# Performance work log

Measured on AMD Instinct MI355X. Metric: run time of the kernel, lower is better.

The kernel has to match this reference:

```python
import jax, jax.numpy as jnp
import numpy as np

DIM = 768
H = 12
HD = DIM // H
SCALE = HD ** (-0.5)


def setup_inputs() -> dict:
    key = jax.random.key(0)
    ks = jax.random.split(key, 10)
    s = DIM ** (-0.5)
    x = jax.random.normal(ks[0], (8, 1024, DIM), dtype=jnp.float32)
    Wq = jax.random.normal(ks[1], (DIM, DIM), dtype=jnp.float32) * s
    Wk = jax.random.normal(ks[2], (DIM, DIM), dtype=jnp.float32) * s
    Wv = jax.random.normal(ks[3], (DIM, DIM), dtype=jnp.float32) * s
    Wl = jax.random.normal(ks[4], (H, H), dtype=jnp.float32) * (H ** -0.5)
    bl = jax.random.normal(ks[5], (H,), dtype=jnp.float32) * 0.02
    Ww = jax.random.normal(ks[6], (H, H), dtype=jnp.float32) * (H ** -0.5)
    bw = jax.random.normal(ks[7], (H,), dtype=jnp.float32) * 0.02
    Wp = jax.random.normal(ks[8], (DIM, DIM), dtype=jnp.float32) * s
    bp = jax.random.normal(ks[9], (DIM,), dtype=jnp.float32) * 0.02
    return {"x": x, "Wq": Wq, "Wk": Wk, "Wv": Wv, "Wl": Wl, "bl": bl,
            "Ww": Ww, "bw": bw, "Wp": Wp, "bp": bp}


def reference(x, Wq, Wk, Wv, Wl, bl, Ww, bw, Wp, bp):
    B, N, C = x.shape
    # QKV projections (no bias), split heads -> (B, H, N, hd)
    q = (x @ Wq).reshape(B, N, H, HD).transpose(0, 2, 1, 3) * SCALE
    k = (x @ Wk).reshape(B, N, H, HD).transpose(0, 2, 1, 3)
    v = (x @ Wv).reshape(B, N, H, HD).transpose(0, 2, 1, 3)
    # scores: (B, H, N, N)
    attn = jnp.einsum('bhid,bhjd->bhij', q, k)
    # talking heads pre-softmax: mix over head axis (Linear on last dim of BNNH)
    attn = jnp.einsum('bhij,gh->bgij', attn, Wl) + bl[None, :, None, None]
    attn = jax.nn.softmax(attn, axis=-1)
    # talking heads post-softmax
    attn = jnp.einsum('bhij,gh->bgij', attn, Ww) + bw[None, :, None, None]
    out = jnp.einsum('bhij,bhjd->bhid', attn, v)  # (B, H, N, hd)
    out = out.transpose(0, 2, 1, 3).reshape(B, N, C)
    return out @ Wp + bp
```

## Files before the change

### kernel.cpp

```cpp
#include <hip/hip_runtime.h>
#include <hip/hip_bf16.h>

#define DIM 768
#define NH 12
#define HD 64
#define SEQ 1024
#define BATCH 8
#define JSPA 4
#define JSPB 2
#define LOG2E 1.44269504f

typedef __bf16 bf16x8 __attribute__((ext_vector_type(8)));
typedef _Float16 f16x4 __attribute__((ext_vector_type(4)));
typedef _Float16 f16x8 __attribute__((ext_vector_type(8)));
typedef float f32x4 __attribute__((ext_vector_type(4)));

__global__ __launch_bounds__(256) void xcvt(
    const float* __restrict__ X, __bf16* __restrict__ Xb)
{
  const size_t i = ((size_t)blockIdx.x * 256 + threadIdx.x) * 8;
  float4 a0 = *(const float4*)(X + i);
  float4 a1 = *(const float4*)(X + i + 4);
  bf16x8 v = { (__bf16)a0.x, (__bf16)a0.y, (__bf16)a0.z, (__bf16)a0.w,
               (__bf16)a1.x, (__bf16)a1.y, (__bf16)a1.z, (__bf16)a1.w };
  *(bf16x8*)(Xb + i) = v;
}

__global__ __launch_bounds__(256) void wtrans(
    const float* __restrict__ Wq, const float* __restrict__ Wk,
    const float* __restrict__ Wv, const float* __restrict__ Wp,
    __bf16* __restrict__ Tq, __bf16* __restrict__ Tk,
    __bf16* __restrict__ Tv, _Float16* __restrict__ Tp)
{
  const int z = blockIdx.z;
  const float* W = (z==0) ? Wq : (z==1) ? Wk : (z==2) ? Wv : Wp;
  __shared__ float tile[32][33];
  const int t = threadIdx.x, tx = t & 31, ty = t >> 5;
  const int k0 = blockIdx.y * 32, n0 = blockIdx.x * 32;
#pragma unroll
  for (int u = 0; u < 4; ++u)
    tile[ty + u*8][tx] = W[(size_t)(k0 + ty + u*8) * DIM + n0 + tx];
  __syncthreads();
  if (z == 3) {
#pragma unroll
    for (int u = 0; u < 4; ++u)
      Tp[(size_t)(n0 + ty + u*8) * DIM + k0 + tx] = (_Float16)tile[tx][ty + u*8];
  } else {
    __bf16* T = (z==0) ? Tq : (z==1) ? Tk : Tv;
#pragma unroll
    for (int u = 0; u < 4; ++u)
      T[(size_t)(n0 + ty + u*8) * DIM + k0 + tx] = (__bf16)tile[tx][ty + u*8];
  }
}

__global__ __launch_bounds__(256) void gemm_qkv(
    const __bf16* __restrict__ Xb, const __bf16* __restrict__ WT,
    __bf16* __restrict__ Qo, __bf16* __restrict__ Ko, _Float16* __restrict__ Vt2)
{
  __shared__ __bf16 As[128 * 40];
  __shared__ __bf16 Bs[128 * 40];

  const int t = threadIdx.x, lane = t & 63, w = t >> 6;
  const int n16 = lane & 15, q = lane >> 4;
  const int m0 = blockIdx.y * 128, n0 = blockIdx.x * 128;
  const int wm = (w >> 1) * 64, wn = (w & 1) * 64;

  const int srow = t >> 2, scol = (t & 3) * 8;
  const __bf16* Ag = Xb + (size_t)(m0 + srow) * DIM + scol;
  const __bf16* Bg = WT + (size_t)(n0 + srow) * DIM + scol;

  f32x4 acc[4][4];
#pragma unroll
  for (int mt = 0; mt < 4; ++mt)
#pragma unroll
    for (int nt = 0; nt < 4; ++nt) acc[mt][nt] = (f32x4){0.f,0.f,0.f,0.f};

  for (int kb = 0; kb < DIM; kb += 32) {
    __syncthreads();
    bf16x8 a0 = *(const bf16x8*)(Ag + kb);
    bf16x8 a1 = *(const bf16x8*)(Ag + (size_t)64 * DIM + kb);
    bf16x8 b0 = *(const bf16x8*)(Bg + kb);
    bf16x8 b1 = *(const bf16x8*)(Bg + (size_t)64 * DIM + kb);
    *(bf16x8*)&As[srow * 40 + scol] = a0;
    *(bf16x8*)&As[(srow + 64) * 40 + scol] = a1;
    *(bf16x8*)&Bs[srow * 40 + scol] = b0;
    *(bf16x8*)&Bs[(srow + 64) * 40 + scol] = b1;
    __syncthreads();

    bf16x8 af[4], bg[4];
#pragma unroll
    for (int mt = 0; mt < 4; ++mt)
      af[mt] = *(const bf16x8*)&As[(wm + mt*16 + n16) * 40 + q*8];
#pragma unroll
    for (int nt = 0; nt < 4; ++nt)
      bg[nt] = *(const bf16x8*)&Bs[(wn + nt*16 + n16) * 40 + q*8];
#pragma unroll
    for (int mt = 0; mt < 4; ++mt)
#pragma unroll
      for (int nt = 0; nt < 4; ++nt)
        acc[mt][nt] = __builtin_amdgcn_mfma_f32_16x16x32_bf16(af[mt], bg[nt], acc[mt][nt], 0, 0, 0);
  }

#pragma unroll
  for (int nt = 0; nt < 4; ++nt) {
    const int n = n0 + wn + nt*16 + n16;
    const int z = n / DIM, c = n % DIM;
    const int h = c >> 6, d = c & 63;
#pragma unroll
    for (int mt = 0; mt < 4; ++mt) {
#pragma unroll
      for (int r = 0; r < 4; ++r) {
        const int row = m0 + wm + mt*16 + q*4 + r;
        const int bb = row >> 10, ii = row & 1023;
        const float v = acc[mt][nt][r];
        if (z == 0)
          Qo[(((size_t)bb*NH + h)*SEQ + ii)*HD + d] = (__bf16)(v * 0.125f);
        else if (z == 1)
          Ko[(((size_t)bb*NH + h)*SEQ + ii)*HD + d] = (__bf16)v;
        else
          Vt2[((((size_t)bb*NH + h)*64 + (ii >> 4))*HD + d)*16 + (ii & 15)] = (_Float16)v;
      }
    }
  }
}

__global__ __launch_bounds__(256) void attn_sums(
    const __bf16* __restrict__ Qg, const __bf16* __restrict__ Kg,
    const float* __restrict__ Wl, const float* __restrict__ bl,
    float* __restrict__ lpart)
{
  __shared__ _Float16 Sl[2][12][324];

  const int t = threadIdx.x, lane = t & 63, w = t >> 6;
  const int n16 = lane & 15, q = lane >> 4;
  const int h0 = w * 3;
  const int b = blockIdx.x, i0 = blockIdx.y * 16, z = blockIdx.z;
  const int jt0 = z * (SEQ/16/JSPA), jt1 = jt0 + SEQ/16/JSPA;
  const size_t bbase = (size_t)b * NH * SEQ * HD;

  f16x4 wlA;
  f32x4 blC;
#pragma unroll
  for (int j = 0; j < 4; ++j) {
    const int k = q*4 + j;
    wlA[j] = (n16 < 12 && k < 12) ? (_Float16)(Wl[n16*12 + k] * LOG2E) : (_Float16)0.f;
    blC[j] = (k < 12) ? bl[k] * LOG2E : 0.f;
  }

  bf16x8 qf[3][2];
#pragma unroll
  for (int hh = 0; hh < 3; ++hh)
#pragma unroll
    for (int cc = 0; cc < 2; ++cc)
      qf[hh][cc] = *(const bf16x8*)(Qg + bbase + ((size_t)(h0+hh)*SEQ + i0 + n16)*HD + cc*32 + q*8);

  const f32x4 z4 = {0.f, 0.f, 0.f, 0.f};

  float lrun[4][4];
#pragma unroll
  for (int c = 0; c < 4; ++c)
#pragma unroll
    for (int r = 0; r < 4; ++r) lrun[c][r] = 0.f;

  bf16x8 kC[3][2], kN[3][2];
#pragma unroll
  for (int hh = 0; hh < 3; ++hh) {
    const __bf16* kp = Kg + bbase + ((size_t)(h0+hh)*SEQ + jt0*16 + n16)*HD + q*8;
    kC[hh][0] = *(const bf16x8*)kp;
    kC[hh][1] = *(const bf16x8*)(kp + 32);
  }

#pragma unroll 2
  for (int jt = jt0; jt < jt1; ++jt) {
    const int buf = jt & 1;
    const int jn = (jt < jt1 - 1) ? jt + 1 : jt;
#pragma unroll
    for (int hh = 0; hh < 3; ++hh) {
      const __bf16* kp = Kg + bbase + ((size_t)(h0+hh)*SEQ + jn*16 + n16)*HD + q*8;
      kN[hh][0] = *(const bf16x8*)kp;
      kN[hh][1] = *(const bf16x8*)(kp + 32);
    }
#pragma unroll
    for (int hh = 0; hh < 3; ++hh) {
      f32x4 s = __builtin_amdgcn_mfma_f32_16x16x32_bf16(kC[hh][0], qf[hh][0], z4, 0, 0, 0);
      s = __builtin_amdgcn_mfma_f32_16x16x32_bf16(kC[hh][1], qf[hh][1], s, 0, 0, 0);
      f16x4 sh = { (_Float16)s[0], (_Float16)s[1], (_Float16)s[2], (_Float16)s[3] };
      *(f16x4*)&Sl[buf][h0+hh][n16*20 + q*4] = sh;
    }
    __syncthreads();
#pragma unroll
    for (int c = 0; c < 4; ++c) {
      const int i = w*4 + c;
      f16x4 sf;
#pragma unroll
      for (int dd = 0; dd < 4; ++dd) {
        int h = q*4 + dd; if (h > 11) h = 11;
        sf[dd] = Sl[buf][h][i*20 + n16];
      }
      f32x4 sm = __builtin_amdgcn_mfma_f32_16x16x16f16(wlA, sf, blC, 0, 0, 0);
#pragma unroll
      for (int r = 0; r < 4; ++r) lrun[c][r] += __builtin_amdgcn_exp2f(sm[r]);
    }
#pragma unroll
    for (int hh = 0; hh < 3; ++hh) { kC[hh][0] = kN[hh][0]; kC[hh][1] = kN[hh][1]; }
  }

  const int tile = b * (SEQ/16) + blockIdx.y;
#pragma unroll
  for (int c = 0; c < 4; ++c) {
#pragma unroll
    for (int r = 0; r < 4; ++r) {
      float l = lrun[c][r];
      l += __shfl_xor(l, 1);
      l += __shfl_xor(l, 2);
      l += __shfl_xor(l, 4);
      l += __shfl_xor(l, 8);
      const int g = q*4 + r;
      if (n16 == 0 && g < 12)
        lpart[(((size_t)tile*JSPA + z)*12 + g)*16 + w*4 + c] = l;
    }
  }
}

__global__ __launch_bounds__(256) void attn_pv(
    const __bf16* __restrict__ Qg, const __bf16* __restrict__ Kg,
    const _Float16* __restrict__ Vt2,
    const float* __restrict__ Wl, const float* __restrict__ bl,
    const float* __restrict__ Ww, const float* __restrict__ bw,
    const float* __restrict__ lpart,
    _Float16* __restrict__ Ap0, _Float16* __restrict__ Ap1)
{
  __shared__ _Float16 Sl[2][12][324];
  __shared__ _Float16 Pl[2][16 * 248];

  const int t = threadIdx.x, lane = t & 63, w = t >> 6;
  const int n16 = lane & 15, q = lane >> 4;
  const int h0 = w * 3;
  const int b = blockIdx.x, i0 = blockIdx.y * 16, z = blockIdx.z;
  const int jt0 = z * (SEQ/16/JSPB), jt1 = jt0 + SEQ/16/JSPB;
  const size_t bbase = (size_t)b * NH * SEQ * HD;

  f16x4 wlA, wwA;
  f32x4 blC, bwC;
#pragma unroll
  for (int j = 0; j < 4; ++j) {
    const int k = q*4 + j;
    wlA[j] = (n16 < 12 && k < 12) ? (_Float16)(Wl[n16*12 + k] * LOG2E) : (_Float16)0.f;
    wwA[j] = (n16 < 12 && k < 12) ? (_Float16)Ww[n16*12 + k] : (_Float16)0.f;
    blC[j] = (k < 12) ? bl[k] * LOG2E : 0.f;
    bwC[j] = (k < 12) ? bw[k] : 0.f;
  }

  const int tile = b * (SEQ/16) + blockIdx.y;
  float linv[4][4];
#pragma unroll
  for (int c = 0; c < 4; ++c)
#pragma unroll
    for (int r = 0; r < 4; ++r) {
      const int g = q*4 + r;
      if (g < 12) {
        float l = 0.f;
#pragma unroll
        for (int zz = 0; zz < JSPA; ++zz)
          l += lpart[(((size_t)tile*JSPA + zz)*12 + g)*16 + w*4 + c];
        linv[c][r] = 1.0f / l;
      } else {
        linv[c][r] = 0.f;
      }
    }

  bf16x8 qf[3][2];
#pragma unroll
  for (int hh = 0; hh < 3; ++hh)
#pragma unroll
    for (int cc = 0; cc < 2; ++cc)
      qf[hh][cc] = *(const bf16x8*)(Qg + bbase + ((size_t)(h0+hh)*SEQ + i0 + n16)*HD + cc*32 + q*8);

  const f32x4 z4 = {0.f, 0.f, 0.f, 0.f};

  f32x4 oacc[3][4];
#pragma unroll
  for (int hh = 0; hh < 3; ++hh)
#pragma unroll
    for (int dc = 0; dc < 4; ++dc) oacc[hh][dc] = z4;

  bf16x8 kC[3][2], kN[3][2];
  f16x4 vC[3][4], vN[3][4];
#pragma unroll
  for (int hh = 0; hh < 3; ++hh) {
    const __bf16* kp = Kg + bbase + ((size_t)(h0+hh)*SEQ + jt0*16 + n16)*HD + q*8;
    kC[hh][0] = *(const bf16x8*)kp;
    kC[hh][1] = *(const bf16x8*)(kp + 32);
  }

#pragma unroll 2
  for (int jt = jt0; jt < jt1; ++jt) {
    const int buf = jt & 1;
    const int jn = (jt < jt1 - 1) ? jt + 1 : jt;
#pragma unroll
    for (int hh = 0; hh < 3; ++hh) {
      const __bf16* kp = Kg + bbase + ((size_t)(h0+hh)*SEQ + jn*16 + n16)*HD + q*8;
      kN[hh][0] = *(const bf16x8*)kp;
      kN[hh][1] = *(const bf16x8*)(kp + 32);
    }
#pragma unroll
    for (int hh = 0; hh < 3; ++hh) {
      const _Float16* vb = Vt2 + (((size_t)(b*NH + h0 + hh)*64 + jt)*HD)*16;
#pragma unroll
      for (int dc = 0; dc < 4; ++dc)
        vN[hh][dc] = *(const f16x4*)(vb + (size_t)(dc*16 + n16)*16 + q*4);
    }
#pragma unroll
    for (int hh = 0; hh < 3; ++hh) {
      f32x4 s = __builtin_amdgcn_mfma_f32_16x16x32_bf16(kC[hh][0], qf[hh][0], z4, 0, 0, 0);
      s = __builtin_amdgcn_mfma_f32_16x16x32_bf16(kC[hh][1], qf[hh][1], s, 0, 0, 0);
      f16x4 sh = { (_Float16)s[0], (_Float16)s[1], (_Float16)s[2], (_Float16)s[3] };
      *(f16x4*)&Sl[buf][h0+hh][n16*20 + q*4] = sh;
    }
    __syncthreads();
#pragma unroll
    for (int c = 0; c < 4; ++c) {
      const int i = w*4 + c;
      f16x4 sf;
#pragma unroll
      for (int dd = 0; dd < 4; ++dd) {
        int h = q*4 + dd; if (h > 11) h = 11;
        sf[dd] = Sl[buf][h][i*20 + n16];
      }
      f32x4 sm = __builtin_amdgcn_mfma_f32_16x16x16f16(wlA, sf, blC, 0, 0, 0);
      f16x4 pnf;
#pragma unroll
      for (int r = 0; r < 4; ++r)
        pnf[r] = (_Float16)(__builtin_amdgcn_exp2f(sm[r]) * linv[c][r]);
      f32x4 p2 = __builtin_amdgcn_mfma_f32_16x16x16f16(wwA, pnf, bwC, 0, 0, 0);
      if (q < 3) {
#pragma unroll
        for (int r = 0; r < 4; ++r)
          Pl[buf][i*248 + (q*4 + r)*20 + n16] = (_Float16)p2[r];
      }
    }
    if (jt > jt0) {
#pragma unroll
      for (int hh = 0; hh < 3; ++hh) {
        const int g2 = h0 + hh;
        f16x4 pa = *(const f16x4*)&Pl[1 - buf][n16*248 + g2*20 + q*4];
#pragma unroll
        for (int dc = 0; dc < 4; ++dc)
          oacc[hh][dc] = __builtin_amdgcn_mfma_f32_16x16x16f16(pa, vC[hh][dc], oacc[hh][dc], 0, 0, 0);
      }
    }
#pragma unroll
    for (int hh = 0; hh < 3; ++hh) {
      kC[hh][0] = kN[hh][0]; kC[hh][1] = kN[hh][1];
#pragma unroll
      for (int dc = 0; dc < 4; ++dc) vC[hh][dc] = vN[hh][dc];
    }
  }
  __syncthreads();
#pragma unroll
  for (int hh = 0; hh < 3; ++hh) {
    const int g2 = h0 + hh;
    f16x4 pa = *(const f16x4*)&Pl[1][n16*248 + g2*20 + q*4];
#pragma unroll
    for (int dc = 0; dc < 4; ++dc)
      oacc[hh][dc] = __builtin_amdgcn_mfma_f32_16x16x16f16(pa, vC[hh][dc], oacc[hh][dc], 0, 0, 0);
  }

  _Float16* Ao = z ? Ap1 : Ap0;
#pragma unroll
  for (int hh = 0; hh < 3; ++hh)
#pragma unroll
    for (int dc = 0; dc < 4; ++dc)
#pragma unroll
      for (int r = 0; r < 4; ++r)
        Ao[((size_t)(b*SEQ + i0 + q*4 + r))*DIM + (h0+hh)*HD + dc*16 + n16] =
            (_Float16)oacc[hh][dc][r];
}

__global__ __launch_bounds__(256) void gemm_proj(
    const _Float16* __restrict__ A0, const _Float16* __restrict__ A1,
    const _Float16* __restrict__ WpT,
    const float* __restrict__ bp, float* __restrict__ Out)
{
  __shared__ _Float16 As[128 * 40];
  __shared__ _Float16 Bs[128 * 40];

  const int t = threadIdx.x, lane = t & 63, w = t >> 6;
  const int n16 = lane & 15, q = lane >> 4;
  const int m0 = blockIdx.y * 128, n0 = blockIdx.x * 128;
  const int wm = (w >> 1) * 64, wn = (w & 1) * 64;

  const int srow = t >> 2, scol = (t & 3) * 8;
  const _Float16* Ag0 = A0 + (size_t)(m0 + srow) * DIM + scol;
  const _Float16* Ag1 = A1 + (size_t)(m0 + srow) * DIM + scol;
  const _Float16* Bg = WpT + (size_t)(n0 + srow) * DIM + scol;

  f32x4 acc[4][4];
#pragma unroll
  for (int nt = 0; nt < 4; ++nt) {
    const float bpv = bp[n0 + wn + nt*16 + n16];
#pragma unroll
    for (int mt = 0; mt < 4; ++mt)
#pragma unroll
      for (int r = 0; r < 4; ++r) acc[mt][nt][r] = bpv;
  }

  for (int kb = 0; kb < DIM; kb += 32) {
    __syncthreads();
    f16x8 a0 = *(const f16x8*)(Ag0 + kb) + *(const f16x8*)(Ag1 + kb);
    f16x8 a1 = *(const f16x8*)(Ag0 + (size_t)64 * DIM + kb) +
               *(const f16x8*)(Ag1 + (size_t)64 * DIM + kb);
    f16x8 b0 = *(const f16x8*)(Bg + kb);
    f16x8 b1 = *(const f16x8*)(Bg + (size_t)64 * DIM + kb);
    *(f16x8*)&As[srow * 40 + scol] = a0;
    *(f16x8*)&As[(srow + 64) * 40 + scol] = a1;
    *(f16x8*)&Bs[srow * 40 + scol] = b0;
    *(f16x8*)&Bs[(srow + 64) * 40 + scol] = b1;
    __syncthreads();

    f16x8 af[4], bg[4];
#pragma unroll
    for (int mt = 0; mt < 4; ++mt)
      af[mt] = *(const f16x8*)&As[(wm + mt*16 + n16) * 40 + q*8];
#pragma unroll
    for (int nt = 0; nt < 4; ++nt)
      bg[nt] = *(const f16x8*)&Bs[(wn + nt*16 + n16) * 40 + q*8];
#pragma unroll
    for (int mt = 0; mt < 4; ++mt)
#pragma unroll
      for (int nt = 0; nt < 4; ++nt)
        acc[mt][nt] = __builtin_amdgcn_mfma_f32_16x16x32_f16(af[mt], bg[nt], acc[mt][nt], 0, 0, 0);
  }

#pragma unroll
  for (int nt = 0; nt < 4; ++nt) {
    const int n = n0 + wn + nt*16 + n16;
#pragma unroll
    for (int mt = 0; mt < 4; ++mt)
#pragma unroll
      for (int r = 0; r < 4; ++r) {
        const int row = m0 + wm + mt*16 + q*4 + r;
        Out[(size_t)row * DIM + n] = acc[mt][nt][r];
      }
  }
}

extern "C" void kernel_launch(void* const* d_in, const int* in_sizes, int n_in,
                              void* d_out, int out_size, void* d_ws, size_t ws_size,
                              hipStream_t stream) {
  const float* x  = (const float*)d_in[0];
  const float* Wq = (const float*)d_in[1];
  const float* Wk = (const float*)d_in[2];
  const float* Wv = (const float*)d_in[3];
  const float* Wl = (const float*)d_in[4];
  const float* bl = (const float*)d_in[5];
  const float* Ww = (const float*)d_in[6];
  const float* bw = (const float*)d_in[7];
  const float* Wp = (const float*)d_in[8];
  const float* bp = (const float*)d_in[9];

  char* p = (char*)d_ws;
  const size_t WSZ = (size_t)DIM * DIM * 2;
  const size_t TSZ = (size_t)BATCH * NH * SEQ * HD * 2;
  const size_t LSZ = (size_t)BATCH * (SEQ/16) * JSPA * 12 * 16 * 4;
  __bf16*   WqT = (__bf16*)p;            p += WSZ;
  __bf16*   WkT = (__bf16*)p;            p += WSZ;
  __bf16*   WvT = (__bf16*)p;            p += WSZ;
  _Float16* WpT = (_Float16*)p;          p += WSZ;
  __bf16*   Q   = (__bf16*)p;            p += TSZ;
  __bf16*   K   = (__bf16*)p;            p += TSZ;
  _Float16* V2  = (_Float16*)p;          p += TSZ;
  _Float16* Ap0 = (_Float16*)p;          p += TSZ;
  __bf16*   Xb  = (__bf16*)p;            p += TSZ;
  float*    lpart = (float*)p;           p += LSZ;
  _Float16* Ap1 = (_Float16*)Xb;

  xcvt<<<dim3((BATCH*SEQ*DIM)/(256*8)), 256, 0, stream>>>(x, Xb);
  wtrans<<<dim3(24, 24, 4), 256, 0, stream>>>(Wq, Wk, Wv, Wp, WqT, WkT, WvT, WpT);
  gemm_qkv<<<dim3(18, 64), 256, 0, stream>>>(Xb, WqT, Q, K, V2);
  attn_sums<<<dim3(BATCH, SEQ/16, JSPA), 256, 0, stream>>>(Q, K, Wl, bl, lpart);
  attn_pv<<<dim3(BATCH, SEQ/16, JSPB), 256, 0, stream>>>(Q, K, V2, Wl, bl, Ww, bw,
                                                         lpart, Ap0, Ap1);
  gemm_proj<<<dim3(6, 64), 256, 0, stream>>>(Ap0, Ap1, WpT, bp, (float*)d_out);
}
```

Before: 521.1 us.

## Software-pipeline attention stages across iterations and drop register prefetch buffers

```diff
diff --git a/kernel.cpp b/kernel.cpp
--- a/kernel.cpp
+++ b/kernel.cpp
@@ -6,7 +6,7 @@
 #define HD 64
 #define SEQ 1024
 #define BATCH 8
-#define JSPA 4
+#define JSPA 2
 #define JSPB 2
 #define LOG2E 1.44269504f
 
@@ -124,7 +124,7 @@
   }
 }
 
-__global__ __launch_bounds__(256) void attn_sums(
+__global__ __launch_bounds__(256, 4) void attn_sums(
     const __bf16* __restrict__ Qg, const __bf16* __restrict__ Kg,
     const float* __restrict__ Wl, const float* __restrict__ bl,
     float* __restrict__ lpart)
@@ -162,23 +162,32 @@
 #pragma unroll
     for (int r = 0; r < 4; ++r) lrun[c][r] = 0.f;
 
-  bf16x8 kC[3][2], kN[3][2];
-#pragma unroll
-  for (int hh = 0; hh < 3; ++hh) {
-    const __bf16* kp = Kg + bbase + ((size_t)(h0+hh)*SEQ + jt0*16 + n16)*HD + q*8;
-    kC[hh][0] = *(const bf16x8*)kp;
-    kC[hh][1] = *(const bf16x8*)(kp + 32);
-  }
+  bf16x8 kC[3][2];
 
 #pragma unroll 2
   for (int jt = jt0; jt < jt1; ++jt) {
     const int buf = jt & 1;
-    const int jn = (jt < jt1 - 1) ? jt + 1 : jt;
-#pragma unroll
-    for (int hh = 0; hh < 3; ++hh) {
-      const __bf16* kp = Kg + bbase + ((size_t)(h0+hh)*SEQ + jn*16 + n16)*HD + q*8;
-      kN[hh][0] = *(const bf16x8*)kp;
-      kN[hh][1] = *(const bf16x8*)(kp + 32);
+#pragma unroll
+    for (int hh = 0; hh < 3; ++hh) {
+      const __bf16* kp = Kg + bbase + ((size_t)(h0+hh)*SEQ + jt*16 + n16)*HD + q*8;
+      kC[hh][0] = *(const bf16x8*)kp;
+      kC[hh][1] = *(const bf16x8*)(kp + 32);
+    }
+    if (jt > jt0) {
+      const int sb = 1 - buf;
+#pragma unroll
+      for (int c = 0; c < 4; ++c) {
+        const int i = w*4 + c;
+        f16x4 sf;
+#pragma unroll
+        for (int dd = 0; dd < 4; ++dd) {
+          int h = q*4 + dd; if (h > 11) h = 11;
+          sf[dd] = Sl[sb][h][i*20 + n16];
+        }
+        f32x4 sm = __builtin_amdgcn_mfma_f32_16x16x16f16(wlA, sf, blC, 0, 0, 0);
+#pragma unroll
+        for (int r = 0; r < 4; ++r) lrun[c][r] += __builtin_amdgcn_exp2f(sm[r]);
+      }
     }
 #pragma unroll
     for (int hh = 0; hh < 3; ++hh) {
@@ -188,6 +197,8 @@
       *(f16x4*)&Sl[buf][h0+hh][n16*20 + q*4] = sh;
     }
     __syncthreads();
+  }
+  {
 #pragma unroll
     for (int c = 0; c < 4; ++c) {
       const int i = w*4 + c;
@@ -195,14 +206,12 @@
 #pragma unroll
       for (int dd = 0; dd < 4; ++dd) {
         int h = q*4 + dd; if (h > 11) h = 11;
-        sf[dd] = Sl[buf][h][i*20 + n16];
+        sf[dd] = Sl[1][h][i*20 + n16];
       }
       f32x4 sm = __builtin_amdgcn_mfma_f32_16x16x16f16(wlA, sf, blC, 0, 0, 0);
 #pragma unroll
       for (int r = 0; r < 4; ++r) lrun[c][r] += __builtin_amdgcn_exp2f(sm[r]);
     }
-#pragma unroll
-    for (int hh = 0; hh < 3; ++hh) { kC[hh][0] = kN[hh][0]; kC[hh][1] = kN[hh][1]; }
   }
 
   const int tile = b * (SEQ/16) + blockIdx.y;
@@ -222,7 +231,7 @@
   }
 }
 
-__global__ __launch_bounds__(256) void attn_pv(
+__global__ __launch_bounds__(256, 4) void attn_pv(
     const __bf16* __restrict__ Qg, const __bf16* __restrict__ Kg,
     const _Float16* __restrict__ Vt2,
     const float* __restrict__ Wl, const float* __restrict__ bl,
@@ -284,31 +293,60 @@
 #pragma unroll
     for (int dc = 0; dc < 4; ++dc) oacc[hh][dc] = z4;
 
-  bf16x8 kC[3][2], kN[3][2];
-  f16x4 vC[3][4], vN[3][4];
-#pragma unroll
-  for (int hh = 0; hh < 3; ++hh) {
-    const __bf16* kp = Kg + bbase + ((size_t)(h0+hh)*SEQ + jt0*16 + n16)*HD + q*8;
-    kC[hh][0] = *(const bf16x8*)kp;
-    kC[hh][1] = *(const bf16x8*)(kp + 32);
-  }
+  bf16x8 kC[3][2];
+  f16x4 vC[3][4];
 
 #pragma unroll 2
   for (int jt = jt0; jt < jt1; ++jt) {
     const int buf = jt & 1;
-    const int jn = (jt < jt1 - 1) ? jt + 1 : jt;
-#pragma unroll
-    for (int hh = 0; hh < 3; ++hh) {
-      const __bf16* kp = Kg + bbase + ((size_t)(h0+hh)*SEQ + jn*16 + n16)*HD + q*8;
-      kN[hh][0] = *(const bf16x8*)kp;
-      kN[hh][1] = *(const bf16x8*)(kp + 32);
-    }
-#pragma unroll
-    for (int hh = 0; hh < 3; ++hh) {
-      const _Float16* vb = Vt2 + (((size_t)(b*NH + h0 + hh)*64 + jt)*HD)*16;
-#pragma unroll
-      for (int dc = 0; dc < 4; ++dc)
-        vN[hh][dc] = *(const f16x4*)(vb + (size_t)(dc*16 + n16)*16 + q*4);
+#pragma unroll
+    for (int hh = 0; hh < 3; ++hh) {
+      const __bf16* kp = Kg + bbase + ((size_t)(h0+hh)*SEQ + jt*16 + n16)*HD + q*8;
+      kC[hh][0] = *(const bf16x8*)kp;
+      kC[hh][1] = *(const bf16x8*)(kp + 32);
+    }
+    if (jt >= jt0 + 2) {
+#pragma unroll
+      for (int hh = 0; hh < 3; ++hh) {
+        const _Float16* vb = Vt2 + (((size_t)(b*NH + h0 + hh)*64 + (jt-2))*HD)*16;
+#pragma unroll
+        for (int dc = 0; dc < 4; ++dc)
+          vC[hh][dc] = *(const f16x4*)(vb + (size_t)(dc*16 + n16)*16 + q*4);
+      }
+    }
+    if (jt > jt0) {
+      const int sb = 1 - buf;
+#pragma unroll
+      for (int c = 0; c < 4; ++c) {
+        const int i = w*4 + c;
+        f16x4 sf;
+#pragma unroll
+        for (int dd = 0; dd < 4; ++dd) {
+          int h = q*4 + dd; if (h > 11) h = 11;
+          sf[dd] = Sl[sb][h][i*20 + n16];
+        }
+        f32x4 sm = __builtin_amdgcn_mfma_f32_16x16x16f16(wlA, sf, blC, 0, 0, 0);
+        f16x4 pnf;
+#pragma unroll
+        for (int r = 0; r < 4; ++r)
+          pnf[r] = (_Float16)(__builtin_amdgcn_exp2f(sm[r]) * linv[c][r]);
+        f32x4 p2 = __builtin_amdgcn_mfma_f32_16x16x16f16(wwA, pnf, bwC, 0, 0, 0);
+        if (q < 3) {
+#pragma unroll
+          for (int r = 0; r < 4; ++r)
+            Pl[buf][i*248 + (q*4 + r)*20 + n16] = (_Float16)p2[r];
+        }
+      }
+    }
+    if (jt >= jt0 + 2) {
+#pragma unroll
+      for (int hh = 0; hh < 3; ++hh) {
+        const int g2 = h0 + hh;
+        f16x4 pa = *(const f16x4*)&Pl[1 - buf][n16*248 + g2*20 + q*4];
+#pragma unroll
+        for (int dc = 0; dc < 4; ++dc)
+          oacc[hh][dc] = __builtin_amdgcn_mfma_f32_16x16x16f16(pa, vC[hh][dc], oacc[hh][dc], 0, 0, 0);
+      }
     }
 #pragma unroll
     for (int hh = 0; hh < 3; ++hh) {
@@ -318,6 +356,16 @@
       *(f16x4*)&Sl[buf][h0+hh][n16*20 + q*4] = sh;
     }
     __syncthreads();
+  }
+
+  {
+#pragma unroll
+    for (int hh = 0; hh < 3; ++hh) {
+      const _Float16* vb = Vt2 + (((size_t)(b*NH + h0 + hh)*64 + (jt1-2))*HD)*16;
+#pragma unroll
+      for (int dc = 0; dc < 4; ++dc)
+        vC[hh][dc] = *(const f16x4*)(vb + (size_t)(dc*16 + n16)*16 + q*4);
+    }
 #pragma unroll
     for (int c = 0; c < 4; ++c) {
       const int i = w*4 + c;
@@ -325,7 +373,7 @@
 #pragma unroll
       for (int dd = 0; dd < 4; ++dd) {
         int h = q*4 + dd; if (h > 11) h = 11;
-        sf[dd] = Sl[buf][h][i*20 + n16];
+        sf[dd] = Sl[1][h][i*20 + n16];
       }
       f32x4 sm = __builtin_amdgcn_mfma_f32_16x16x16f16(wlA, sf, blC, 0, 0, 0);
       f16x4 pnf;
@@ -336,34 +384,33 @@
       if (q < 3) {
 #pragma unroll
         for (int r = 0; r < 4; ++r)
-          Pl[buf][i*248 + (q*4 + r)*20 + n16] = (_Float16)p2[r];
-      }
-    }
-    if (jt > jt0) {
-#pragma unroll
-      for (int hh = 0; hh < 3; ++hh) {
-        const int g2 = h0 + hh;
-        f16x4 pa = *(const f16x4*)&Pl[1 - buf][n16*248 + g2*20 + q*4];
-#pragma unroll
-        for (int dc = 0; dc < 4; ++dc)
-          oacc[hh][dc] = __builtin_amdgcn_mfma_f32_16x16x16f16(pa, vC[hh][dc], oacc[hh][dc], 0, 0, 0);
-      }
-    }
-#pragma unroll
-    for (int hh = 0; hh < 3; ++hh) {
-      kC[hh][0] = kN[hh][0]; kC[hh][1] = kN[hh][1];
-#pragma unroll
-      for (int dc = 0; dc < 4; ++dc) vC[hh][dc] = vN[hh][dc];
-    }
-  }
-  __syncthreads();
-#pragma unroll
-  for (int hh = 0; hh < 3; ++hh) {
-    const int g2 = h0 + hh;
-    f16x4 pa = *(const f16x4*)&Pl[1][n16*248 + g2*20 + q*4];
-#pragma unroll
-    for (int dc = 0; dc < 4; ++dc)
-      oacc[hh][dc] = __builtin_amdgcn_mfma_f32_16x16x16f16(pa, vC[hh][dc], oacc[hh][dc], 0, 0, 0);
+          Pl[0][i*248 + (q*4 + r)*20 + n16] = (_Float16)p2[r];
+      }
+    }
+#pragma unroll
+    for (int hh = 0; hh < 3; ++hh) {
+      const int g2 = h0 + hh;
+      f16x4 pa = *(const f16x4*)&Pl[1][n16*248 + g2*20 + q*4];
+#pragma unroll
+      for (int dc = 0; dc < 4; ++dc)
+        oacc[hh][dc] = __builtin_amdgcn_mfma_f32_16x16x16f16(pa, vC[hh][dc], oacc[hh][dc], 0, 0, 0);
+    }
+#pragma unroll
+    for (int hh = 0; hh < 3; ++hh) {
+      const _Float16* vb = Vt2 + (((size_t)(b*NH + h0 + hh)*64 + (jt1-1))*HD)*16;
+#pragma unroll
+      for (int dc = 0; dc < 4; ++dc)
+        vC[hh][dc] = *(const f16x4*)(vb + (size_t)(dc*16 + n16)*16 + q*4);
+    }
+    __syncthreads();
+#pragma unroll
+    for (int hh = 0; hh < 3; ++hh) {
+      const int g2 = h0 + hh;
+      f16x4 pa = *(const f16x4*)&Pl[0][n16*248 + g2*20 + q*4];
+#pragma unroll
+      for (int dc = 0; dc < 4; ++dc)
+        oacc[hh][dc] = __builtin_amdgcn_mfma_f32_16x16x16f16(pa, vC[hh][dc], oacc[hh][dc], 0, 0, 0);
+    }
   }
 
   _Float16* Ao = z ? Ap1 : Ap0;
```

Measured after the change: 887.6 us. 1.7x slower.
